# Kernel optimization log

Measured on AMD Instinct MI355X. Metric: run time of the kernel, lower is better.

## Reference

```python
import jax, jax.numpy as jnp
import numpy as np

NHEADS = 16
NGROUPS = 16
NEG = -1e9

def _apply_rope(t, cos, sin):
    # t: (B,T,H,hs) -> pairs (B,T,H,hs//2,2); complex multiply by (cos + i*sin)
    B, T, H, hs = t.shape
    tp = t.reshape(B, T, H, hs // 2, 2)
    a, b = tp[..., 0], tp[..., 1]
    c = cos[None, :, None, :]
    s = sin[None, :, None, :]
    out = jnp.stack([a * c - b * s, a * s + b * c], axis=-1)
    return out.reshape(B, T, H, hs)

def _causal_attn(q, k, v):
    # q,k: (..., S, d); v: (..., S, dv); causal softmax attention, scale 1/sqrt(d)
    d = q.shape[-1]
    S = q.shape[-2]
    scores = jnp.einsum('...qd,...kd->...qk', q, k) / jnp.sqrt(jnp.asarray(d, q.dtype))
    mask = jnp.tril(jnp.ones((S, S), dtype=bool))
    scores = jnp.where(mask, scores, NEG)
    p = jax.nn.softmax(scores, axis=-1)
    return jnp.einsum('...qk,...kd->...qd', p, v)

def setup_inputs() -> dict:
    key = jax.random.key(0)
    k1, k2, k3 = jax.random.split(key, 3)
    B, T, C = 4, 2048, 1024
    hs = C // NHEADS
    x = jax.random.normal(k1, (B, T, C), dtype=jnp.float32)
    w_attn = jax.random.normal(k2, (3 * C, C), dtype=jnp.float32) * (1.0 / np.sqrt(C))
    w_proj = jax.random.normal(k3, (C, C), dtype=jnp.float32) * (1.0 / np.sqrt(C))
    # standard RoPE frequencies: theta_i = 10000^{-2i/hs}
    inv = 1.0 / (10000.0 ** (np.arange(0, hs, 2, dtype=np.float32) / hs))  # (hs//2,)
    ang = np.arange(T, dtype=np.float32)[:, None] * inv[None, :]           # (T, hs//2)
    freqs_cos = jnp.asarray(np.cos(ang), dtype=jnp.float32)
    freqs_sin = jnp.asarray(np.sin(ang), dtype=jnp.float32)
    return {'x': x, 'w_attn': w_attn, 'w_proj': w_proj,
            'freqs_cos': freqs_cos, 'freqs_sin': freqs_sin}

def reference(x, w_attn, w_proj, freqs_cos, freqs_sin):
    B, T, C = x.shape
    H = NHEADS
    hs = C // H
    G = min(T // (T // NGROUPS), NGROUPS)  # group_t = block_size // ngroups, T == block_size
    Tg = T // G
    qkv = x @ w_attn.T                      # (B,T,3C)
    q, k, v = jnp.split(qkv, 3, axis=2)
    # RoPE
    q = _apply_rope(q.reshape(B, T, H, hs), freqs_cos, freqs_sin).reshape(B, T, C)
    k = _apply_rope(k.reshape(B, T, H, hs), freqs_cos, freqs_sin).reshape(B, T, C)
    # group: (B, G, Tg, H, hs) -> (B, H, G, Tg, hs)
    def grp(t):
        return t.reshape(B, G, Tg, H, hs).transpose(0, 3, 1, 2, 4)
    q, k, v = grp(q), grp(k), grp(v)
    # its_time branch: append mean-pooled summary token per group
    q = jnp.concatenate([q, q.mean(axis=3, keepdims=True)], axis=3)  # (B,H,G,Tg+1,hs)
    k = jnp.concatenate([k, k.mean(axis=3, keepdims=True)], axis=3)
    v = jnp.concatenate([v, v.mean(axis=3, keepdims=True)], axis=3)
    att = _causal_attn(q, k, v)             # (B,H,G,Tg+1,hs)
    # group-level attention over summary tokens of all but last group
    q2 = q[:, :, :-1, -1]                   # (B,H,G-1,hs)
    k2 = k[:, :, :-1, -1]
    av = att[:, :, :-1, -1]                 # (B,H,G-1,hs)
    v2 = _causal_attn(q2, k2, av)           # (B,H,G-1,hs)
    y_q = q2[:, :, :, None, :]              # (B,H,G-1,1,hs)
    y_k = k2[:, :, :, None, :]
    y_v = v2[:, :, :, None, :]
    # drop summary tokens, merge groups back: (B,H,G,Tg,hs) -> (B,T,C)
    xo = att[:, :, :, :-1]
    xo = xo.reshape(B, H, T, hs).transpose(0, 2, 1, 3).reshape(B, T, C)
    out = xo @ w_proj.T
    return (out, y_q, y_k, y_v)
```

## Files before the change

kernel.cpp:

```cpp
#include <hip/hip_runtime.h>
#include <hip/hip_bf16.h>

#define HS 64
#define NH 16
#define NG 16
#define TT 2048
#define CC 1024
#define BBATCH 4
#define TG 128
#define SS 129

typedef __attribute__((ext_vector_type(8))) short bf16x8;
typedef __attribute__((ext_vector_type(4))) float f32x4;

__device__ __forceinline__ float bf2f(ushort u) {
  return __uint_as_float(((unsigned)u) << 16);
}
__device__ __forceinline__ ushort f2bf(float f) {
  unsigned x = __float_as_uint(f);
  x += 0x7fff + ((x >> 16) & 1);
  return (ushort)(x >> 16);
}
__device__ __forceinline__ bf16x8 mk8(ushort4 a0, ushort4 a1) {
  bf16x8 v;
  v[0] = (short)a0.x; v[1] = (short)a0.y; v[2] = (short)a0.z; v[3] = (short)a0.w;
  v[4] = (short)a1.x; v[5] = (short)a1.y; v[6] = (short)a1.z; v[7] = (short)a1.w;
  return v;
}

__global__ void cvt3(const float* __restrict__ x, const float* __restrict__ wa,
                     const float* __restrict__ wp, ushort* __restrict__ xb,
                     ushort* __restrict__ wab, ushort* __restrict__ wpb) {
  const int stride = gridDim.x * blockDim.x;
  for (int i = blockIdx.x * blockDim.x + threadIdx.x; i < 3145728; i += stride) {
    const float* src; ushort* dst; int off;
    if (i < 2097152) { src = x; dst = xb; off = i; }
    else if (i < 2883584) { src = wa; dst = wab; off = i - 2097152; }
    else { src = wp; dst = wpb; off = i - 2883584; }
    float4 v = ((const float4*)src)[off];
    ushort4 o;
    o.x = f2bf(v.x); o.y = f2bf(v.y); o.z = f2bf(v.z); o.w = f2bf(v.w);
    ((ushort4*)dst)[off] = o;
  }
}

template <bool OUT_BF16>
__global__ __launch_bounds__(256) void gemm_bt(const ushort* __restrict__ A,
                                               const ushort* __restrict__ Bw,
                                               void* __restrict__ Cout,
                                               int M, int N, int K) {
  __shared__ ushort As[128][68];
  __shared__ ushort Bs[128][68];
  const int m0 = blockIdx.y * 128;
  const int n0 = blockIdx.x * 128;
  const int tid = threadIdx.x;
  const int lane = tid & 63;
  const int wv = tid >> 6;
  const int wr = wv >> 1, wc = wv & 1;
  const int lo = lane & 15, hi = lane >> 4;

  f32x4 acc[4][4];
#pragma unroll
  for (int i = 0; i < 4; ++i)
#pragma unroll
    for (int j = 0; j < 4; ++j) acc[i][j] = (f32x4)0.0f;

  for (int k0 = 0; k0 < K; k0 += 64) {
    __syncthreads();
#pragma unroll
    for (int t = 0; t < 4; ++t) {
      int c = tid + 256 * t;
      int row = c >> 3, cc = c & 7;
      uint4 va = *(const uint4*)(A + (size_t)(m0 + row) * K + k0 + cc * 8);
      *(uint2*)&As[row][cc * 8]     = make_uint2(va.x, va.y);
      *(uint2*)&As[row][cc * 8 + 4] = make_uint2(va.z, va.w);
      uint4 vb = *(const uint4*)(Bw + (size_t)(n0 + row) * K + k0 + cc * 8);
      *(uint2*)&Bs[row][cc * 8]     = make_uint2(vb.x, vb.y);
      *(uint2*)&Bs[row][cc * 8 + 4] = make_uint2(vb.z, vb.w);
    }
    __syncthreads();
#pragma unroll
    for (int kk = 0; kk < 64; kk += 32) {
      bf16x8 af[4], bfr[4];
#pragma unroll
      for (int i = 0; i < 4; ++i) {
        int r = wr * 64 + i * 16 + lo;
        af[i] = mk8(*(const ushort4*)&As[r][kk + 4 * hi],
                    *(const ushort4*)&As[r][kk + 16 + 4 * hi]);
      }
#pragma unroll
      for (int j = 0; j < 4; ++j) {
        int r = wc * 64 + j * 16 + lo;
        bfr[j] = mk8(*(const ushort4*)&Bs[r][kk + 4 * hi],
                     *(const ushort4*)&Bs[r][kk + 16 + 4 * hi]);
      }
#pragma unroll
      for (int i = 0; i < 4; ++i)
#pragma unroll
        for (int j = 0; j < 4; ++j)
          acc[i][j] = __builtin_amdgcn_mfma_f32_16x16x32_bf16(af[i], bfr[j], acc[i][j], 0, 0, 0);
    }
  }
#pragma unroll
  for (int i = 0; i < 4; ++i) {
    int row = m0 + wr * 64 + i * 16 + 4 * hi;
#pragma unroll
    for (int j = 0; j < 4; ++j) {
      int col = n0 + wc * 64 + j * 16 + lo;
#pragma unroll
      for (int r = 0; r < 4; ++r) {
        float v = acc[i][j][r];
        if constexpr (OUT_BF16) {
          ((ushort*)Cout)[(size_t)(row + r) * N + col] = f2bf(v);
        } else {
          ((float*)Cout)[(size_t)(row + r) * N + col] = v;
        }
      }
    }
  }
}

__global__ __launch_bounds__(512, 4) void attn1f(const ushort* __restrict__ qkv,
                                                 const float* __restrict__ fc,
                                                 const float* __restrict__ fs,
                                                 ushort* __restrict__ xo, float* __restrict__ attm,
                                                 float* __restrict__ yq, float* __restrict__ yk) {
  __shared__ ushort qs[144][68];
  __shared__ ushort ks[144][68];
  __shared__ ushort vt[64][148];
  __shared__ ushort obuf[8][16][68];
  float (*redL)[8][24] = reinterpret_cast<float(*)[8][24]>(&obuf[0][0][0]);
  const int blk = blockIdx.x;
  const int g = blk & 15, h = (blk >> 4) & 15, b = blk >> 8;
  const int tid = threadIdx.x;
  const int lane = tid & 63, wv = tid >> 6;
  const int lo = lane & 15, hi = lane >> 4;

  if (tid < 320) {
    int d = tid / 5, ch = (tid % 5) * 4;
    *(ushort4*)&vt[d][128 + ch] = make_ushort4(0, 0, 0, 0);
  }

  const size_t rowbase = (size_t)(b * TT + g * TG) * (3 * CC) + h * HS;
  const int srow = tid >> 3;
  const int c8 = (tid & 7) * 8;
  float msq[8], msk[8], msv[8];
#pragma unroll
  for (int j = 0; j < 8; ++j) { msq[j] = 0.f; msk[j] = 0.f; msv[j] = 0.f; }
#pragma unroll
  for (int it = 0; it < 6; ++it) {
    const int part = it >> 1;
    const int s = srow + 64 * (it & 1);
    uint4 w = *(const uint4*)(qkv + rowbase + (size_t)s * (3 * CC) + part * CC + c8);
    ushort e[8];
    *(uint4*)e = w;
    if (part == 2) {
#pragma unroll
      for (int j = 0; j < 8; ++j) { msv[j] += bf2f(e[j]); vt[c8 + j][s] = e[j]; }
    } else {
      const int ts = g * TG + s;
      float4 cv = *(const float4*)&fc[ts * 32 + (c8 >> 1)];
      float4 sv = *(const float4*)&fs[ts * 32 + (c8 >> 1)];
      float a0 = bf2f(e[0]), a1 = bf2f(e[1]), a2 = bf2f(e[2]), a3 = bf2f(e[3]);
      float a4 = bf2f(e[4]), a5 = bf2f(e[5]), a6 = bf2f(e[6]), a7 = bf2f(e[7]);
      float r0 = a0 * cv.x - a1 * sv.x, r1 = a0 * sv.x + a1 * cv.x;
      float r2 = a2 * cv.y - a3 * sv.y, r3 = a2 * sv.y + a3 * cv.y;
      float r4 = a4 * cv.z - a5 * sv.z, r5 = a4 * sv.z + a5 * cv.z;
      float r6 = a6 * cv.w - a7 * sv.w, r7 = a6 * sv.w + a7 * cv.w;
      uint4 o;
      o.x = (unsigned)f2bf(r0) | ((unsigned)f2bf(r1) << 16);
      o.y = (unsigned)f2bf(r2) | ((unsigned)f2bf(r3) << 16);
      o.z = (unsigned)f2bf(r4) | ((unsigned)f2bf(r5) << 16);
      o.w = (unsigned)f2bf(r6) | ((unsigned)f2bf(r7) << 16);
      if (part == 0) {
        *(uint4*)&qs[s][c8] = o;
        msq[0] += r0; msq[1] += r1; msq[2] += r2; msq[3] += r3;
        msq[4] += r4; msq[5] += r5; msq[6] += r6; msq[7] += r7;
      } else {
        *(uint4*)&ks[s][c8] = o;
        msk[0] += r0; msk[1] += r1; msk[2] += r2; msk[3] += r3;
        msk[4] += r4; msk[5] += r5; msk[6] += r6; msk[7] += r7;
      }
    }
  }
#pragma unroll
  for (int j = 0; j < 8; ++j) {
    msq[j] += __shfl_xor(msq[j], 8); msq[j] += __shfl_xor(msq[j], 16); msq[j] += __shfl_xor(msq[j], 32);
    msk[j] += __shfl_xor(msk[j], 8); msk[j] += __shfl_xor(msk[j], 16); msk[j] += __shfl_xor(msk[j], 32);
    msv[j] += __shfl_xor(msv[j], 8); msv[j] += __shfl_xor(msv[j], 16); msv[j] += __shfl_xor(msv[j], 32);
  }
  if (lane < 8) {
#pragma unroll
    for (int j = 0; j < 8; ++j) {
      redL[wv][lane][j] = msq[j];
      redL[wv][lane][8 + j] = msk[j];
      redL[wv][lane][16 + j] = msv[j];
    }
  }
  __syncthreads();
  if (tid < 64) {
    const int cg = tid >> 3, j = tid & 7;
    float mq = 0.f, mk2 = 0.f, mv = 0.f;
#pragma unroll
    for (int w = 0; w < 8; ++w) {
      mq += redL[w][cg][j];
      mk2 += redL[w][cg][8 + j];
      mv += redL[w][cg][16 + j];
    }
    mq *= (1.0f / 128.0f); mk2 *= (1.0f / 128.0f); mv *= (1.0f / 128.0f);
    qs[128][tid] = f2bf(mq);
    ks[128][tid] = f2bf(mk2);
    vt[tid][128] = f2bf(mv);
    if (g < 15) {
      size_t yo = ((size_t)(b * 16 + h) * 15 + g) * 64 + tid;
      yq[yo] = mq; yk[yo] = mk2;
    }
  }
  __syncthreads();

#pragma unroll
  for (int ti = 0; ti < 2; ++ti) {
    const int t = (ti == 0) ? (8 - wv) : ((wv == 7) ? 0 : -1);
    if (t < 0) continue;
    const int q0 = t * 16;

    bf16x8 bq[2];
#pragma unroll
    for (int k2 = 0; k2 < 2; ++k2)
      bq[k2] = mk8(*(const ushort4*)&qs[q0 + lo][k2 * 32 + 4 * hi],
                   *(const ushort4*)&qs[q0 + lo][k2 * 32 + 16 + 4 * hi]);

    f32x4 sc[9];
#pragma unroll
    for (int n = 0; n < 9; ++n) sc[n] = (f32x4)0.0f;
#pragma unroll
    for (int n = 0; n < 9; ++n) {
      if (n > t) continue;
#pragma unroll
      for (int k2 = 0; k2 < 2; ++k2) {
        bf16x8 ak = mk8(*(const ushort4*)&ks[n * 16 + lo][k2 * 32 + 4 * hi],
                        *(const ushort4*)&ks[n * 16 + lo][k2 * 32 + 16 + 4 * hi]);
        sc[n] = __builtin_amdgcn_mfma_f32_16x16x32_bf16(ak, bq[k2], sc[n], 0, 0, 0);
      }
    }

    const int qi = q0 + lo;
    float mx = -INFINITY;
#pragma unroll
    for (int n = 0; n < 9; ++n) {
      if (n > t) continue;
#pragma unroll
      for (int r = 0; r < 4; ++r) {
        int kj = n * 16 + 4 * hi + r;
        float v = (kj <= qi) ? sc[n][r] * 0.125f : -INFINITY;
        sc[n][r] = v;
        mx = fmaxf(mx, v);
      }
    }
    mx = fmaxf(mx, __shfl_xor(mx, 16));
    mx = fmaxf(mx, __shfl_xor(mx, 32));
    float sum = 0.f;
#pragma unroll
    for (int n = 0; n < 9; ++n) {
      if (n > t) continue;
#pragma unroll
      for (int r = 0; r < 4; ++r) {
        float e = __expf(sc[n][r] - mx);
        sc[n][r] = e;
        sum += e;
      }
    }
    sum += __shfl_xor(sum, 16);
    sum += __shfl_xor(sum, 32);
    const float inv = 1.0f / sum;

    f32x4 oac[4];
#pragma unroll
    for (int m = 0; m < 4; ++m) oac[m] = (f32x4)0.0f;
#pragma unroll
    for (int s2 = 0; s2 < 5; ++s2) {
      if (s2 > (t >> 1)) continue;
      const int kt1ok = (2 * s2 + 1 <= t);
      bf16x8 pb;
#pragma unroll
      for (int e = 0; e < 4; ++e) pb[e] = (short)f2bf(sc[2 * s2][e] * inv);
      if (kt1ok) {
#pragma unroll
        for (int e = 0; e < 4; ++e) pb[e + 4] = (short)f2bf(sc[2 * s2 + 1][e] * inv);
      } else {
#pragma unroll
        for (int e = 0; e < 4; ++e) pb[e + 4] = 0;
      }
#pragma unroll
      for (int m = 0; m < 4; ++m) {
        ushort4 a0 = *(const ushort4*)&vt[m * 16 + lo][32 * s2 + 4 * hi];
        ushort4 a1 = kt1ok ? *(const ushort4*)&vt[m * 16 + lo][32 * s2 + 16 + 4 * hi]
                           : make_ushort4(0, 0, 0, 0);
        oac[m] = __builtin_amdgcn_mfma_f32_16x16x32_bf16(mk8(a0, a1), pb, oac[m], 0, 0, 0);
      }
    }

    if (t < 8) {
#pragma unroll
      for (int m = 0; m < 4; ++m)
#pragma unroll
        for (int r = 0; r < 4; ++r)
          obuf[wv][lo][m * 16 + 4 * hi + r] = f2bf(oac[m][r]);
#pragma unroll
      for (int it = 0; it < 4; ++it) {
        int idx = lane + 64 * it;
        int r = idx >> 4;
        int c4 = (idx & 15) * 4;
        uint2 val = *(const uint2*)&obuf[wv][r][c4];
        int tok = g * TG + t * 16 + r;
        *(uint2*)(xo + ((size_t)(b * TT + tok)) * CC + h * HS + c4) = val;
      }
    } else {
      if (lo == 0) {
#pragma unroll
        for (int m = 0; m < 4; ++m)
#pragma unroll
          for (int r = 0; r < 4; ++r)
            attm[(size_t)blk * 64 + m * 16 + 4 * hi + r] = oac[m][r];
      }
    }
  }
}

__global__ __launch_bounds__(64) void attn2(const float* __restrict__ yq,
                                            const float* __restrict__ yk,
                                            const float* __restrict__ attm,
                                            float* __restrict__ yv) {
  __shared__ float qs2[15][64], ks2[15][64], avs[15][64], srow[16];
  int bh = blockIdx.x, lane = threadIdx.x;
  for (int j = 0; j < 15; ++j) {
    qs2[j][lane] = yq[((size_t)bh * 15 + j) * 64 + lane];
    ks2[j][lane] = yk[((size_t)bh * 15 + j) * 64 + lane];
    avs[j][lane] = attm[((size_t)bh * 16 + j) * 64 + lane];
  }
  __syncthreads();
  for (int i = 0; i < 15; ++i) {
    float qv = qs2[i][lane];
    for (int j = 0; j <= i; ++j) {
      float t = qv * ks2[j][lane];
#pragma unroll
      for (int off = 32; off > 0; off >>= 1) t += __shfl_xor(t, off);
      if (lane == 0) srow[j] = t * 0.125f;
    }
    __syncthreads();
    float mx = -INFINITY;
    for (int j = 0; j <= i; ++j) mx = fmaxf(mx, srow[j]);
    float den = 0;
    for (int j = 0; j <= i; ++j) den += __expf(srow[j] - mx);
    float inv = 1.0f / den;
    float o = 0;
    for (int j = 0; j <= i; ++j) o += __expf(srow[j] - mx) * inv * avs[j][lane];
    yv[((size_t)bh * 15 + i) * 64 + lane] = o;
    __syncthreads();
  }
}

extern "C" void kernel_launch(void* const* d_in, const int* in_sizes, int n_in,
                              void* d_out, int out_size, void* d_ws, size_t ws_size,
                              hipStream_t stream) {
  const float* x      = (const float*)d_in[0];
  const float* w_attn = (const float*)d_in[1];
  const float* w_proj = (const float*)d_in[2];
  const float* fc     = (const float*)d_in[3];
  const float* fs     = (const float*)d_in[4];
  float* out = (float*)d_out;

  char* ws = (char*)d_ws;
  ushort* xb   = (ushort*)(ws);
  ushort* xo   = (ushort*)(ws);
  ushort* wab  = (ushort*)(ws + 16777216);
  float*  attm = (float*) (ws + 16777216);
  ushort* wpb  = (ushort*)(ws + 23068672);
  ushort* qkv  = (ushort*)(ws + 25165824);

  float* yq = out + 8388608;
  float* yk = out + 8450048;
  float* yv = out + 8511488;

  cvt3<<<2048, 256, 0, stream>>>(x, w_attn, w_proj, xb, wab, wpb);
  gemm_bt<true><<<dim3(24, 64), 256, 0, stream>>>(xb, wab, qkv, 8192, 3072, 1024);
  attn1f<<<1024, 512, 0, stream>>>(qkv, fc, fs, xo, attm, yq, yk);
  attn2<<<64, 64, 0, stream>>>(yq, yk, attm, yv);
  gemm_bt<false><<<dim3(8, 64), 256, 0, stream>>>(xo, wpb, out, 8192, 1024, 1024);
}
```

Measured before the change: 177.0 us.

## Rewrite GEMMs with triple-buffered direct global-to-LDS loads and 256x128 tiles

Replaces the register-staged, single-buffered bf16 GEMM with a triple-buffered pipeline that uses global_load_lds to copy tiles straight into shared memory, overlapping the load of tile t+2 with MFMA work on tile t. Block tile grows to 256x128 with 512 threads (8 waves), and LDS fragments are read as contiguous 16-byte vectors. The aim is to hide global memory latency and drop the per-iteration double barrier and register round-trip. In exchange, the unpadded LDS layout may cause bank conflicts, the LDS footprint per block is larger, and K is hardcoded to 1024.

```diff
diff --git a/kernel.cpp b/kernel.cpp
--- a/kernel.cpp
+++ b/kernel.cpp
@@ -26,6 +26,10 @@
   v[0] = (short)a0.x; v[1] = (short)a0.y; v[2] = (short)a0.z; v[3] = (short)a0.w;
   v[4] = (short)a1.x; v[5] = (short)a1.y; v[6] = (short)a1.z; v[7] = (short)a1.w;
   return v;
+}
+__device__ __forceinline__ void load_lds16(const ushort* g, ushort* l) {
+  __builtin_amdgcn_global_load_lds((const __attribute__((address_space(1))) unsigned int*)g,
+                                   (__attribute__((address_space(3))) unsigned int*)l, 16, 0, 0);
 }
 
 __global__ void cvt3(const float* __restrict__ x, const float* __restrict__ wa,
@@ -45,19 +49,21 @@
 }
 
 template <bool OUT_BF16>
-__global__ __launch_bounds__(256) void gemm_bt(const ushort* __restrict__ A,
+__global__ __launch_bounds__(512) void gemm_p3(const ushort* __restrict__ A,
                                                const ushort* __restrict__ Bw,
-                                               void* __restrict__ Cout,
-                                               int M, int N, int K) {
-  __shared__ ushort As[128][68];
-  __shared__ ushort Bs[128][68];
-  const int m0 = blockIdx.y * 128;
+                                               void* __restrict__ Cout, int N) {
+  const int Kd = 1024;
+  const int nt = 16;
+  __shared__ ushort lds[3 * 384 * 64];
+  const int m0 = blockIdx.y * 256;
   const int n0 = blockIdx.x * 128;
   const int tid = threadIdx.x;
   const int lane = tid & 63;
-  const int wv = tid >> 6;
-  const int wr = wv >> 1, wc = wv & 1;
+  const int w = tid >> 6;
+  const int wm = w >> 1, wn = w & 1;
   const int lo = lane & 15, hi = lane >> 4;
+  const int rb = tid >> 3;
+  const int c8 = (tid & 7) * 8;
 
   f32x4 acc[4][4];
 #pragma unroll
@@ -65,48 +71,64 @@
 #pragma unroll
     for (int j = 0; j < 4; ++j) acc[i][j] = (f32x4)0.0f;
 
-  for (int k0 = 0; k0 < K; k0 += 64) {
-    __syncthreads();
-#pragma unroll
-    for (int t = 0; t < 4; ++t) {
-      int c = tid + 256 * t;
-      int row = c >> 3, cc = c & 7;
-      uint4 va = *(const uint4*)(A + (size_t)(m0 + row) * K + k0 + cc * 8);
-      *(uint2*)&As[row][cc * 8]     = make_uint2(va.x, va.y);
-      *(uint2*)&As[row][cc * 8 + 4] = make_uint2(va.z, va.w);
-      uint4 vb = *(const uint4*)(Bw + (size_t)(n0 + row) * K + k0 + cc * 8);
-      *(uint2*)&Bs[row][cc * 8]     = make_uint2(vb.x, vb.y);
-      *(uint2*)&Bs[row][cc * 8 + 4] = make_uint2(vb.z, vb.w);
-    }
-    __syncthreads();
+#define STG(tt, buf)                                                              \
+  {                                                                               \
+    ushort* dstb = lds + (buf) * 24576 + w * 512;                                 \
+    const int k0s = (tt) * 64;                                                    \
+    load_lds16(A + (size_t)(m0 + rb) * Kd + k0s + c8,        dstb);               \
+    load_lds16(A + (size_t)(m0 + 64 + rb) * Kd + k0s + c8,   dstb + 4096);        \
+    load_lds16(A + (size_t)(m0 + 128 + rb) * Kd + k0s + c8,  dstb + 8192);        \
+    load_lds16(A + (size_t)(m0 + 192 + rb) * Kd + k0s + c8,  dstb + 12288);       \
+    load_lds16(Bw + (size_t)(n0 + rb) * Kd + k0s + c8,       dstb + 16384);       \
+    load_lds16(Bw + (size_t)(n0 + 64 + rb) * Kd + k0s + c8,  dstb + 20480);       \
+  }
+
+  STG(0, 0)
+  STG(1, 1)
+  asm volatile("s_waitcnt vmcnt(6)" ::: "memory");
+  __builtin_amdgcn_s_barrier();
+
+  int cur = 0;
+  for (int t = 0; t < nt; ++t) {
+    if (t + 2 < nt) {
+      const int nb = (cur == 0) ? 2 : (cur - 1);
+      STG(t + 2, nb)
+    }
+    const ushort* Ac = lds + cur * 24576;
+    const ushort* Bc = Ac + 16384;
 #pragma unroll
     for (int kk = 0; kk < 64; kk += 32) {
       bf16x8 af[4], bfr[4];
 #pragma unroll
-      for (int i = 0; i < 4; ++i) {
-        int r = wr * 64 + i * 16 + lo;
-        af[i] = mk8(*(const ushort4*)&As[r][kk + 4 * hi],
-                    *(const ushort4*)&As[r][kk + 16 + 4 * hi]);
-      }
-#pragma unroll
-      for (int j = 0; j < 4; ++j) {
-        int r = wc * 64 + j * 16 + lo;
-        bfr[j] = mk8(*(const ushort4*)&Bs[r][kk + 4 * hi],
-                     *(const ushort4*)&Bs[r][kk + 16 + 4 * hi]);
-      }
+      for (int i = 0; i < 4; ++i)
+        af[i] = *(const bf16x8*)(Ac + (wm * 64 + i * 16 + lo) * 64 + kk + 8 * hi);
+#pragma unroll
+      for (int j = 0; j < 4; ++j)
+        bfr[j] = *(const bf16x8*)(Bc + (wn * 64 + j * 16 + lo) * 64 + kk + 8 * hi);
 #pragma unroll
       for (int i = 0; i < 4; ++i)
 #pragma unroll
         for (int j = 0; j < 4; ++j)
           acc[i][j] = __builtin_amdgcn_mfma_f32_16x16x32_bf16(af[i], bfr[j], acc[i][j], 0, 0, 0);
     }
-  }
+    if (t + 1 < nt) {
+      if (t + 2 < nt) {
+        asm volatile("s_waitcnt vmcnt(6)" ::: "memory");
+      } else {
+        asm volatile("s_waitcnt vmcnt(0)" ::: "memory");
+      }
+      __builtin_amdgcn_s_barrier();
+      cur = (cur == 2) ? 0 : (cur + 1);
+    }
+  }
+#undef STG
+
 #pragma unroll
   for (int i = 0; i < 4; ++i) {
-    int row = m0 + wr * 64 + i * 16 + 4 * hi;
+    int row = m0 + wm * 64 + i * 16 + 4 * hi;
 #pragma unroll
     for (int j = 0; j < 4; ++j) {
-      int col = n0 + wc * 64 + j * 16 + lo;
+      int col = n0 + wn * 64 + j * 16 + lo;
 #pragma unroll
       for (int r = 0; r < 4; ++r) {
         float v = acc[i][j][r];
@@ -383,8 +405,8 @@
   float* yv = out + 8511488;
 
   cvt3<<<2048, 256, 0, stream>>>(x, w_attn, w_proj, xb, wab, wpb);
-  gemm_bt<true><<<dim3(24, 64), 256, 0, stream>>>(xb, wab, qkv, 8192, 3072, 1024);
+  gemm_p3<true><<<dim3(24, 32), 512, 0, stream>>>(xb, wab, qkv, 3072);
   attn1f<<<1024, 512, 0, stream>>>(qkv, fc, fs, xo, attm, yq, yk);
   attn2<<<64, 64, 0, stream>>>(yq, yk, attm, yv);
-  gemm_bt<false><<<dim3(8, 64), 256, 0, stream>>>(xo, wpb, out, 8192, 1024, 1024);
-}
+  gemm_p3<false><<<dim3(8, 32), 512, 0, stream>>>(xo, wpb, out, 1024);
+}
```

Result: no change. 177.2 us (+0.2%).
